# Performance work log

Hardware: AMD Instinct MI355X
Metric: run time of the kernel (lower is better)

The kernel has to match this reference:

```python
import jax, jax.numpy as jnp
import numpy as np
import math

BS, C, NH, NL, NP = 2, 128, 1, 2, 8
SHAPES = np.array([[128, 256], [64, 128]], dtype=np.int64)  # [num_level, (H, W)]
NQ = int(SHAPES[0, 0] * SHAPES[0, 1])  # 32768 queries at level-0 resolution
NV = int((SHAPES[:, 0] * SHAPES[:, 1]).sum())  # 40960


def _offset_bias():
    # replicate init_weights grid bias
    thetas = np.arange(NH, dtype=np.float32) * (2.0 * math.pi / NH)
    grid = np.stack([np.cos(thetas), np.sin(thetas)], -1)
    grid = grid / np.abs(grid).max(-1, keepdims=True)
    grid = np.tile(grid.reshape(NH, 1, 1, 2), (1, NL, NP, 1))
    for i in range(NP):
        grid[:, :, i, :] *= i + 1
    return jnp.asarray(grid.reshape(-1), dtype=jnp.float32)


def setup_inputs() -> dict:
    key = jax.random.key(0)
    ks = jax.random.split(key, 8)
    query = jax.random.normal(ks[0], (BS, NQ, C), dtype=jnp.float32)
    value = jax.random.normal(ks[1], (BS, NV, C), dtype=jnp.float32)
    query_location = jax.random.uniform(ks[2], (BS, NQ, NL, 2), dtype=jnp.float32)
    spatial_shapes = jnp.asarray(SHAPES)
    level_start_index = jnp.asarray(np.concatenate([[0], np.cumsum(SHAPES[:, 0] * SHAPES[:, 1])[:-1]]))
    # params (small random offset weights instead of exact-zero init so offsets depend on query)
    W_off = 0.01 * jax.random.normal(ks[3], (C, NH * NL * NP * 2), dtype=jnp.float32)
    b_off = _offset_bias()
    W_attn = 0.01 * jax.random.normal(ks[4], (C, NH * NL * NP), dtype=jnp.float32)
    b_attn = jnp.zeros((NH * NL * NP,), dtype=jnp.float32)
    lim = 1.0 / np.sqrt(C)
    W_out = jax.random.uniform(ks[5], (C * NH, C), minval=-lim, maxval=lim, dtype=jnp.float32)
    b_out = jnp.zeros((C,), dtype=jnp.float32)
    return {"query": query, "value": value, "query_location": query_location,
            "spatial_shapes": spatial_shapes, "level_start_index": level_start_index,
            "W_off": W_off, "b_off": b_off, "W_attn": W_attn, "b_attn": b_attn,
            "W_out": W_out, "b_out": b_out}


def _ms_deform_attn(value, shapes_np, loc, aw):
    # value: [bs, nv, c]; loc: [bs, nq, nh, nl, np, 2] in [0,1]; aw: [bs, nq, nh, nl, np]
    bs, nq = loc.shape[0], loc.shape[1]
    hd = value.shape[-1] // NH
    out = jnp.zeros((bs, NH, nq, hd), dtype=value.dtype)
    start = 0
    for l in range(NL):
        H, W = int(shapes_np[l, 0]), int(shapes_np[l, 1])
        # [bs, nh, H*W, hd]
        v = value[:, start:start + H * W].reshape(bs, H * W, NH, hd).transpose(0, 2, 1, 3)
        # grid_sample align_corners=False convention: x = gx*W - 0.5 with gx in [0,1]
        x = loc[:, :, :, l, :, 0] * W - 0.5  # [bs, nq, nh, np]
        y = loc[:, :, :, l, :, 1] * H - 0.5
        x0 = jnp.floor(x); y0 = jnp.floor(y)
        lx = (x - x0).transpose(0, 2, 1, 3).reshape(bs, NH, nq * NP)[..., None]
        ly = (y - y0).transpose(0, 2, 1, 3).reshape(bs, NH, nq * NP)[..., None]
        x0i = x0.astype(jnp.int32); y0i = y0.astype(jnp.int32)

        def gat(ix, iy):
            valid = ((ix >= 0) & (ix < W) & (iy >= 0) & (iy < H)).astype(value.dtype)
            idx = jnp.clip(iy, 0, H - 1) * W + jnp.clip(ix, 0, W - 1)
            idx_t = idx.transpose(0, 2, 1, 3).reshape(bs, NH, nq * NP)
            g = jnp.take_along_axis(v, idx_t[..., None], axis=2)  # [bs, nh, nq*np, hd]
            m = valid.transpose(0, 2, 1, 3).reshape(bs, NH, nq * NP)
            return g * m[..., None]

        samp = (gat(x0i, y0i) * (1 - lx) * (1 - ly)
                + gat(x0i + 1, y0i) * lx * (1 - ly)
                + gat(x0i, y0i + 1) * (1 - lx) * ly
                + gat(x0i + 1, y0i + 1) * lx * ly)  # [bs, nh, nq*np, hd]
        w = aw[:, :, :, l].transpose(0, 2, 1, 3).reshape(bs, NH, nq * NP)[..., None]
        out = out + (samp * w).reshape(bs, NH, nq, NP, hd).sum(3)
        start += H * W
    return out.transpose(0, 2, 1, 3).reshape(bs, nq, NH * hd)


def reference(query, value, query_location, spatial_shapes, level_start_index,
              W_off, b_off, W_attn, b_attn, W_out, b_out):
    bs, nq, c = query.shape
    shapes_np = np.asarray(spatial_shapes)
    off = (query @ W_off + b_off).reshape(bs, nq, NH, NL, NP, 2)
    aw = jax.nn.softmax((query @ W_attn + b_attn).reshape(bs, nq, NH, NL * NP), axis=-1)
    aw = aw.reshape(bs, nq, NH, NL, NP)
    # offset_normalizer = [W, H] per level
    norm = jnp.stack([jnp.asarray(shapes_np[:, 1], jnp.float32),
                      jnp.asarray(shapes_np[:, 0], jnp.float32)], -1)  # [nl, 2]
    loc = query_location[:, :, None, :, None, :] + off / norm[None, None, None, :, None, :]
    out = _ms_deform_attn(value, shapes_np, loc, aw)
    return out @ W_out + b_out  # dropout is identity at eval
```

## Files before the change

### kernel.cpp

```cpp
#include <hip/hip_runtime.h>


#define QB 32

__global__ __launch_bounds__(256, 4) void msda_gather_kernel(
    const float* __restrict__ query,
    const float* __restrict__ value,
    const float* __restrict__ qloc,
    const float* __restrict__ Woff,
    const float* __restrict__ boff,
    const float* __restrict__ Wattn,
    const float* __restrict__ battn,
    float* __restrict__ acc_out)
{
    __shared__ __align__(16) char smem_u[QB * 128 * 4];
    __shared__ float coords[QB * 32];
    __shared__ float aws[QB * 16];

    float*  q_tile = (float*)smem_u;
    float4* wo_w   = (float4*)smem_u;
    int4*   wo_o   = (int4*)(smem_u + QB * 16 * 16);

    const int tid = threadIdx.x;
    const int r0  = blockIdx.x * QB;

    {
        const float4* src = (const float4*)query + (size_t)r0 * 32;
        float4* dst = (float4*)q_tile;
        #pragma unroll
        for (int i = 0; i < 4; ++i)
            dst[tid + i * 256] = src[tid + i * 256];
    }
    __syncthreads();

    {
        const int jo = tid & 31;
        const int qb = (tid >> 5) * 4;
        float s[4] = {0.f, 0.f, 0.f, 0.f};
        for (int c4 = 0; c4 < 32; ++c4) {
            const float w0 = Woff[(c4 * 4 + 0) * 32 + jo];
            const float w1 = Woff[(c4 * 4 + 1) * 32 + jo];
            const float w2 = Woff[(c4 * 4 + 2) * 32 + jo];
            const float w3 = Woff[(c4 * 4 + 3) * 32 + jo];
            #pragma unroll
            for (int k = 0; k < 4; ++k) {
                const float4 q4 = *(const float4*)&q_tile[(qb + k) * 128 + c4 * 4];
                s[k] += q4.x * w0 + q4.y * w1 + q4.z * w2 + q4.w * w3;
            }
        }
        const int l = jo >> 4;
        const int d = jo & 1;
        const float scale = (d == 0) ? (l == 0 ? 256.f : 128.f)
                                     : (l == 0 ? 128.f : 64.f);
        const float bo = boff[jo];
        #pragma unroll
        for (int k = 0; k < 4; ++k) {
            const int row = r0 + qb + k;
            const float ql = qloc[row * 4 + l * 2 + d];
            coords[(qb + k) * 32 + jo] = ql * scale + (s[k] + bo) - 0.5f;
        }
    }

    {
        const int ja = tid & 15;
        const int qb = (tid >> 4) * 2;
        float s[2] = {0.f, 0.f};
        for (int c4 = 0; c4 < 32; ++c4) {
            const float w0 = Wattn[(c4 * 4 + 0) * 16 + ja];
            const float w1 = Wattn[(c4 * 4 + 1) * 16 + ja];
            const float w2 = Wattn[(c4 * 4 + 2) * 16 + ja];
            const float w3 = Wattn[(c4 * 4 + 3) * 16 + ja];
            #pragma unroll
            for (int k = 0; k < 2; ++k) {
                const float4 q4 = *(const float4*)&q_tile[(qb + k) * 128 + c4 * 4];
                s[k] += q4.x * w0 + q4.y * w1 + q4.z * w2 + q4.w * w3;
            }
        }
        const float ba = battn[ja];
        #pragma unroll
        for (int k = 0; k < 2; ++k)
            aws[(qb + k) * 16 + ja] = s[k] + ba;
    }
    __syncthreads();

    if (tid < QB) {
        float* a = &aws[tid * 16];
        float m = a[0];
        #pragma unroll
        for (int j = 1; j < 16; ++j) m = fmaxf(m, a[j]);
        float sum = 0.f;
        #pragma unroll
        for (int j = 0; j < 16; ++j) {
            const float e = __expf(a[j] - m);
            a[j] = e;
            sum += e;
        }
        const float r = 1.f / sum;
        #pragma unroll
        for (int j = 0; j < 16; ++j) a[j] *= r;
    }
    __syncthreads();

    #pragma unroll
    for (int e = tid; e < QB * 16; e += 256) {
        const int q = e >> 4;
        const int p = e & 15;
        const int l = p >> 3;
        const int H = l ? 64 : 128;
        const int W = l ? 128 : 256;
        const int S = l ? 32768 : 0;
        const float x   = coords[q * 32 + p * 2 + 0];
        const float y   = coords[q * 32 + p * 2 + 1];
        const float wgt = aws[q * 16 + p];
        const float xf = floorf(x), yf = floorf(y);
        const float lx = x - xf, ly = y - yf;
        const int x0 = (int)xf, y0 = (int)yf;
        const int x1 = x0 + 1, y1 = y0 + 1;
        const float hx = 1.f - lx, hy = 1.f - ly;
        float w00 = wgt * hx * hy;
        float w10 = wgt * lx * hy;
        float w01 = wgt * hx * ly;
        float w11 = wgt * lx * ly;
        if (x0 < 0 || x0 >= W) { w00 = 0.f; w01 = 0.f; }
        if (x1 < 0 || x1 >= W) { w10 = 0.f; w11 = 0.f; }
        if (y0 < 0 || y0 >= H) { w00 = 0.f; w10 = 0.f; }
        if (y1 < 0 || y1 >= H) { w01 = 0.f; w11 = 0.f; }
        const int cx0 = min(max(x0, 0), W - 1);
        const int cx1 = min(max(x1, 0), W - 1);
        const int cy0 = min(max(y0, 0), H - 1);
        const int cy1 = min(max(y1, 0), H - 1);
        wo_w[e] = make_float4(w00, w10, w01, w11);
        wo_o[e] = make_int4((S + cy0 * W + cx0) * 32,
                            (S + cy0 * W + cx1) * 32,
                            (S + cy1 * W + cx0) * 32,
                            (S + cy1 * W + cx1) * 32);
    }
    __syncthreads();

    {
        const int wv   = tid >> 6;
        const int lane = tid & 63;
        const int half = lane >> 5;
        const int cl   = lane & 31;
        const float4* vb = (const float4*)value
                         + (size_t)(blockIdx.x >> 10) * (40960 * 32);
        float4* og = (float4*)acc_out;

        #pragma unroll 1
        for (int i = 0; i < 8; ++i) {
            const int q = wv * 8 + i;
            const int base_e = q * 16;
            float ax = 0.f, ay = 0.f, az = 0.f, aw4 = 0.f;

            #pragma unroll 1
            for (int p0 = 0; p0 < 16; p0 += 8) {
                int   oa[8], ob[8];
                float wa[8], wb[8];
                #pragma unroll
                for (int pi = 0; pi < 8; ++pi) {
                    const float4 w = wo_w[base_e + p0 + pi];
                    const int4   o = wo_o[base_e + p0 + pi];
                    oa[pi] = (half ? o.y : o.x) + cl;
                    ob[pi] = (half ? o.w : o.z) + cl;
                    wa[pi] = half ? w.y : w.x;
                    wb[pi] = half ? w.w : w.z;
                }
                float4 vA[8], vB[8];
                #pragma unroll
                for (int pi = 0; pi < 8; ++pi) {
                    vA[pi] = vb[oa[pi]];
                    vB[pi] = vb[ob[pi]];
                }
                #pragma unroll
                for (int pi = 0; pi < 8; ++pi) {
                    ax  += wa[pi] * vA[pi].x + wb[pi] * vB[pi].x;
                    ay  += wa[pi] * vA[pi].y + wb[pi] * vB[pi].y;
                    az  += wa[pi] * vA[pi].z + wb[pi] * vB[pi].z;
                    aw4 += wa[pi] * vA[pi].w + wb[pi] * vB[pi].w;
                }
            }
            ax  += __shfl_xor(ax, 32, 64);
            ay  += __shfl_xor(ay, 32, 64);
            az  += __shfl_xor(az, 32, 64);
            aw4 += __shfl_xor(aw4, 32, 64);
            if (half == 0)
                og[(size_t)(r0 + q) * 32 + cl] = make_float4(ax, ay, az, aw4);
        }
    }
}

#define GR 64

__global__ __launch_bounds__(256, 3) void msda_out_gemm_kernel(
    const float* __restrict__ Wout,
    const float* __restrict__ bout,
    float* __restrict__ out)
{
    __shared__ __align__(16) float a_tile[GR * 68];
    __shared__ __align__(16) float w_tile[64 * 128];
    const int tid  = threadIdx.x;
    const int r0   = blockIdx.x * GR;
    const int trow = tid >> 4;
    const int tcol = tid & 15;

    float4 o[4][2];
    #pragma unroll
    for (int k = 0; k < 4; ++k) {
        o[k][0] = make_float4(0.f, 0.f, 0.f, 0.f);
        o[k][1] = make_float4(0.f, 0.f, 0.f, 0.f);
    }

    #pragma unroll 1
    for (int h = 0; h < 2; ++h) {
        {
            const float4* src = (const float4*)out;
            #pragma unroll
            for (int i = 0; i < 4; ++i) {
                const int t  = tid + i * 256;
                const int r  = t >> 4;
                const int c4 = t & 15;
                const float4 v = src[(size_t)(r0 + r) * 32 + h * 16 + c4];
                *(float4*)&a_tile[r * 68 + c4 * 4] = v;
            }
            const float4* ws = (const float4*)Wout + (size_t)h * 64 * 32;
            float4* wd = (float4*)w_tile;
            #pragma unroll
            for (int i = 0; i < 8; ++i)
                wd[tid + i * 256] = ws[tid + i * 256];
        }
        __syncthreads();

        #pragma unroll 1
        for (int c4 = 0; c4 < 16; ++c4) {
            float4 a4[4];
            #pragma unroll
            for (int k = 0; k < 4; ++k)
                a4[k] = *(const float4*)&a_tile[(trow + 16 * k) * 68 + c4 * 4];
            #pragma unroll
            for (int j = 0; j < 4; ++j) {
                const int ci = c4 * 4 + j;
                const float4 w0 = *(const float4*)&w_tile[ci * 128 + tcol * 8];
                const float4 w1 = *(const float4*)&w_tile[ci * 128 + tcol * 8 + 4];
                #pragma unroll
                for (int k = 0; k < 4; ++k) {
                    const float a = (j == 0) ? a4[k].x : (j == 1) ? a4[k].y
                                  : (j == 2) ? a4[k].z : a4[k].w;
                    o[k][0].x += a * w0.x; o[k][0].y += a * w0.y;
                    o[k][0].z += a * w0.z; o[k][0].w += a * w0.w;
                    o[k][1].x += a * w1.x; o[k][1].y += a * w1.y;
                    o[k][1].z += a * w1.z; o[k][1].w += a * w1.w;
                }
            }
        }
        __syncthreads();
    }

    const float4 b0 = ((const float4*)bout)[tcol * 2];
    const float4 b1 = ((const float4*)bout)[tcol * 2 + 1];
    float4* og = (float4*)out;
    #pragma unroll
    for (int k = 0; k < 4; ++k) {
        const size_t row = (size_t)(r0 + trow + 16 * k);
        float4 v0 = o[k][0], v1 = o[k][1];
        v0.x += b0.x; v0.y += b0.y; v0.z += b0.z; v0.w += b0.w;
        v1.x += b1.x; v1.y += b1.y; v1.z += b1.z; v1.w += b1.w;
        og[row * 32 + tcol * 2]     = v0;
        og[row * 32 + tcol * 2 + 1] = v1;
    }
}

extern "C" void kernel_launch(void* const* d_in, const int* in_sizes, int n_in,
                              void* d_out, int out_size, void* d_ws, size_t ws_size,
                              hipStream_t stream) {
    const float* query = (const float*)d_in[0];
    const float* value = (const float*)d_in[1];
    const float* qloc  = (const float*)d_in[2];
    const float* Woff  = (const float*)d_in[5];
    const float* boff  = (const float*)d_in[6];
    const float* Wattn = (const float*)d_in[7];
    const float* battn = (const float*)d_in[8];
    const float* Wout  = (const float*)d_in[9];
    const float* bout  = (const float*)d_in[10];
    float* out = (float*)d_out;

    hipLaunchKernelGGL(msda_gather_kernel, dim3(65536 / QB), dim3(256), 0, stream,
                       query, value, qloc, Woff, boff, Wattn, battn, out);
    hipLaunchKernelGGL(msda_out_gemm_kernel, dim3(65536 / GR), dim3(256), 0, stream,
                       Wout, bout, out);
}
```

Measured before the change: 274.8 us.

## Convert value tensor to fp16 in workspace and gather half-precision samples

Adds a pre-pass kernel that converts the value tensor to fp16 in the workspace. A new gather kernel reads 8-byte half4 samples instead of 16-byte float4, and issues all 16 points' loads up front before accumulating in fp32. The goal is to halve gather bandwidth and cache footprint and to improve memory-level parallelism. It costs an extra conversion pass over the value tensor each call, adds fp16 rounding error, and raises register pressure. The old fp32 path is kept as a fallback when the workspace is too small.

```diff
diff --git a/kernel.cpp b/kernel.cpp
--- a/kernel.cpp
+++ b/kernel.cpp
@@ -1,9 +1,207 @@
 #include <hip/hip_runtime.h>
+#include <hip/hip_fp16.h>
 
 
 #define QB 32
 
-__global__ __launch_bounds__(256, 4) void msda_gather_kernel(
+struct __align__(8) h2x2 { __half2 a, b; };
+
+__global__ __launch_bounds__(256) void cvt_value_f16_kernel(
+    const float4* __restrict__ in, h2x2* __restrict__ out, int n4)
+{
+    const int i = blockIdx.x * 256 + threadIdx.x;
+    if (i < n4) {
+        const float4 f = in[i];
+        h2x2 h;
+        h.a = __floats2half2_rn(f.x, f.y);
+        h.b = __floats2half2_rn(f.z, f.w);
+        out[i] = h;
+    }
+}
+
+#define MSDA_PROLOGUE                                                          \
+    float*  q_tile = (float*)smem_u;                                           \
+    float4* wo_w   = (float4*)smem_u;                                          \
+    int4*   wo_o   = (int4*)(smem_u + QB * 16 * 16);                           \
+    const int tid = threadIdx.x;                                               \
+    const int r0  = blockIdx.x * QB;                                           \
+    {                                                                          \
+        const float4* src = (const float4*)query + (size_t)r0 * 32;            \
+        float4* dst = (float4*)q_tile;                                         \
+        _Pragma("unroll")                                                      \
+        for (int i = 0; i < 4; ++i)                                            \
+            dst[tid + i * 256] = src[tid + i * 256];                           \
+    }                                                                          \
+    __syncthreads();                                                           \
+    {                                                                          \
+        const int jo = tid & 31;                                               \
+        const int qb = (tid >> 5) * 4;                                         \
+        float s[4] = {0.f, 0.f, 0.f, 0.f};                                     \
+        for (int c4 = 0; c4 < 32; ++c4) {                                      \
+            const float w0 = Woff[(c4 * 4 + 0) * 32 + jo];                     \
+            const float w1 = Woff[(c4 * 4 + 1) * 32 + jo];                     \
+            const float w2 = Woff[(c4 * 4 + 2) * 32 + jo];                     \
+            const float w3 = Woff[(c4 * 4 + 3) * 32 + jo];                     \
+            _Pragma("unroll")                                                  \
+            for (int k = 0; k < 4; ++k) {                                      \
+                const float4 q4 = *(const float4*)&q_tile[(qb + k) * 128 + c4 * 4]; \
+                s[k] += q4.x * w0 + q4.y * w1 + q4.z * w2 + q4.w * w3;         \
+            }                                                                  \
+        }                                                                      \
+        const int l = jo >> 4;                                                 \
+        const int d = jo & 1;                                                  \
+        const float scale = (d == 0) ? (l == 0 ? 256.f : 128.f)                \
+                                     : (l == 0 ? 128.f : 64.f);                \
+        const float bo = boff[jo];                                             \
+        _Pragma("unroll")                                                      \
+        for (int k = 0; k < 4; ++k) {                                          \
+            const int row = r0 + qb + k;                                       \
+            const float ql = qloc[row * 4 + l * 2 + d];                        \
+            coords[(qb + k) * 32 + jo] = ql * scale + (s[k] + bo) - 0.5f;      \
+        }                                                                      \
+    }                                                                          \
+    {                                                                          \
+        const int ja = tid & 15;                                               \
+        const int qb = (tid >> 4) * 2;                                         \
+        float s[2] = {0.f, 0.f};                                               \
+        for (int c4 = 0; c4 < 32; ++c4) {                                      \
+            const float w0 = Wattn[(c4 * 4 + 0) * 16 + ja];                    \
+            const float w1 = Wattn[(c4 * 4 + 1) * 16 + ja];                    \
+            const float w2 = Wattn[(c4 * 4 + 2) * 16 + ja];                    \
+            const float w3 = Wattn[(c4 * 4 + 3) * 16 + ja];                    \
+            _Pragma("unroll")                                                  \
+            for (int k = 0; k < 2; ++k) {                                      \
+                const float4 q4 = *(const float4*)&q_tile[(qb + k) * 128 + c4 * 4]; \
+                s[k] += q4.x * w0 + q4.y * w1 + q4.z * w2 + q4.w * w3;         \
+            }                                                                  \
+        }                                                                      \
+        const float ba = battn[ja];                                            \
+        _Pragma("unroll")                                                      \
+        for (int k = 0; k < 2; ++k)                                            \
+            aws[(qb + k) * 16 + ja] = s[k] + ba;                               \
+    }                                                                          \
+    __syncthreads();                                                           \
+    if (tid < QB) {                                                            \
+        float* a = &aws[tid * 16];                                             \
+        float m = a[0];                                                        \
+        _Pragma("unroll")                                                      \
+        for (int j = 1; j < 16; ++j) m = fmaxf(m, a[j]);                       \
+        float sum = 0.f;                                                       \
+        _Pragma("unroll")                                                      \
+        for (int j = 0; j < 16; ++j) {                                         \
+            const float e = __expf(a[j] - m);                                  \
+            a[j] = e;                                                          \
+            sum += e;                                                          \
+        }                                                                      \
+        const float r = 1.f / sum;                                             \
+        _Pragma("unroll")                                                      \
+        for (int j = 0; j < 16; ++j) a[j] *= r;                                \
+    }                                                                          \
+    __syncthreads();                                                           \
+    _Pragma("unroll")                                                          \
+    for (int e = tid; e < QB * 16; e += 256) {                                 \
+        const int q = e >> 4;                                                  \
+        const int p = e & 15;                                                  \
+        const int l = p >> 3;                                                  \
+        const int H = l ? 64 : 128;                                            \
+        const int W = l ? 128 : 256;                                           \
+        const int S = l ? 32768 : 0;                                           \
+        const float x   = coords[q * 32 + p * 2 + 0];                          \
+        const float y   = coords[q * 32 + p * 2 + 1];                          \
+        const float wgt = aws[q * 16 + p];                                     \
+        const float xf = floorf(x), yf = floorf(y);                            \
+        const float lx = x - xf, ly = y - yf;                                  \
+        const int x0 = (int)xf, y0 = (int)yf;                                  \
+        const int x1 = x0 + 1, y1 = y0 + 1;                                    \
+        const float hx = 1.f - lx, hy = 1.f - ly;                              \
+        float w00 = wgt * hx * hy;                                             \
+        float w10 = wgt * lx * hy;                                             \
+        float w01 = wgt * hx * ly;                                             \
+        float w11 = wgt * lx * ly;                                             \
+        if (x0 < 0 || x0 >= W) { w00 = 0.f; w01 = 0.f; }                       \
+        if (x1 < 0 || x1 >= W) { w10 = 0.f; w11 = 0.f; }                       \
+        if (y0 < 0 || y0 >= H) { w00 = 0.f; w10 = 0.f; }                       \
+        if (y1 < 0 || y1 >= H) { w01 = 0.f; w11 = 0.f; }                       \
+        const int cx0 = min(max(x0, 0), W - 1);                                \
+        const int cx1 = min(max(x1, 0), W - 1);                                \
+        const int cy0 = min(max(y0, 0), H - 1);                                \
+        const int cy1 = min(max(y1, 0), H - 1);                                \
+        wo_w[e] = make_float4(w00, w10, w01, w11);                             \
+        wo_o[e] = make_int4((S + cy0 * W + cx0) * 32,                          \
+                            (S + cy0 * W + cx1) * 32,                          \
+                            (S + cy1 * W + cx0) * 32,                          \
+                            (S + cy1 * W + cx1) * 32);                        \
+    }                                                                          \
+    __syncthreads();
+
+__global__ __launch_bounds__(256, 4) void msda_gather_f16_kernel(
+    const float* __restrict__ query,
+    const h2x2*  __restrict__ value_h,
+    const float* __restrict__ qloc,
+    const float* __restrict__ Woff,
+    const float* __restrict__ boff,
+    const float* __restrict__ Wattn,
+    const float* __restrict__ battn,
+    float* __restrict__ acc_out)
+{
+    __shared__ __align__(16) char smem_u[QB * 128 * 4];
+    __shared__ float coords[QB * 32];
+    __shared__ float aws[QB * 16];
+    MSDA_PROLOGUE
+
+    {
+        const int wv   = tid >> 6;
+        const int lane = tid & 63;
+        const int half = lane >> 5;
+        const int cl   = lane & 31;
+        const h2x2* vb = value_h + (size_t)(blockIdx.x >> 10) * (40960 * 32);
+        float4* og = (float4*)acc_out;
+
+        #pragma unroll 1
+        for (int i = 0; i < 8; ++i) {
+            const int q = wv * 8 + i;
+            const int base_e = q * 16;
+            float ax = 0.f, ay = 0.f, az = 0.f, aw4 = 0.f;
+
+            int   oa[16], ob[16];
+            float wa[16], wb[16];
+            #pragma unroll
+            for (int p = 0; p < 16; ++p) {
+                const float4 w = wo_w[base_e + p];
+                const int4   o = wo_o[base_e + p];
+                oa[p] = (half ? o.y : o.x) + cl;
+                ob[p] = (half ? o.w : o.z) + cl;
+                wa[p] = half ? w.y : w.x;
+                wb[p] = half ? w.w : w.z;
+            }
+            h2x2 vA[16], vB[16];
+            #pragma unroll
+            for (int p = 0; p < 16; ++p) {
+                vA[p] = vb[oa[p]];
+                vB[p] = vb[ob[p]];
+            }
+            #pragma unroll
+            for (int p = 0; p < 16; ++p) {
+                const float2 a0 = __half22float2(vA[p].a);
+                const float2 a1 = __half22float2(vA[p].b);
+                const float2 b0 = __half22float2(vB[p].a);
+                const float2 b1 = __half22float2(vB[p].b);
+                ax  += wa[p] * a0.x + wb[p] * b0.x;
+                ay  += wa[p] * a0.y + wb[p] * b0.y;
+                az  += wa[p] * a1.x + wb[p] * b1.x;
+                aw4 += wa[p] * a1.y + wb[p] * b1.y;
+            }
+            ax  += __shfl_xor(ax, 32, 64);
+            ay  += __shfl_xor(ay, 32, 64);
+            az  += __shfl_xor(az, 32, 64);
+            aw4 += __shfl_xor(aw4, 32, 64);
+            if (half == 0)
+                og[(size_t)(r0 + q) * 32 + cl] = make_float4(ax, ay, az, aw4);
+        }
+    }
+}
+
+__global__ __launch_bounds__(256, 4) void msda_gather_f32_kernel(
     const float* __restrict__ query,
     const float* __restrict__ value,
     const float* __restrict__ qloc,
@@ -16,126 +214,7 @@
     __shared__ __align__(16) char smem_u[QB * 128 * 4];
     __shared__ float coords[QB * 32];
     __shared__ float aws[QB * 16];
-
-    float*  q_tile = (float*)smem_u;
-    float4* wo_w   = (float4*)smem_u;
-    int4*   wo_o   = (int4*)(smem_u + QB * 16 * 16);
-
-    const int tid = threadIdx.x;
-    const int r0  = blockIdx.x * QB;
-
-    {
-        const float4* src = (const float4*)query + (size_t)r0 * 32;
-        float4* dst = (float4*)q_tile;
-        #pragma unroll
-        for (int i = 0; i < 4; ++i)
-            dst[tid + i * 256] = src[tid + i * 256];
-    }
-    __syncthreads();
-
-    {
-        const int jo = tid & 31;
-        const int qb = (tid >> 5) * 4;
-        float s[4] = {0.f, 0.f, 0.f, 0.f};
-        for (int c4 = 0; c4 < 32; ++c4) {
-            const float w0 = Woff[(c4 * 4 + 0) * 32 + jo];
-            const float w1 = Woff[(c4 * 4 + 1) * 32 + jo];
-            const float w2 = Woff[(c4 * 4 + 2) * 32 + jo];
-            const float w3 = Woff[(c4 * 4 + 3) * 32 + jo];
-            #pragma unroll
-            for (int k = 0; k < 4; ++k) {
-                const float4 q4 = *(const float4*)&q_tile[(qb + k) * 128 + c4 * 4];
-                s[k] += q4.x * w0 + q4.y * w1 + q4.z * w2 + q4.w * w3;
-            }
-        }
-        const int l = jo >> 4;
-        const int d = jo & 1;
-        const float scale = (d == 0) ? (l == 0 ? 256.f : 128.f)
-                                     : (l == 0 ? 128.f : 64.f);
-        const float bo = boff[jo];
-        #pragma unroll
-        for (int k = 0; k < 4; ++k) {
-            const int row = r0 + qb + k;
-            const float ql = qloc[row * 4 + l * 2 + d];
-            coords[(qb + k) * 32 + jo] = ql * scale + (s[k] + bo) - 0.5f;
-        }
-    }
-
-    {
-        const int ja = tid & 15;
-        const int qb = (tid >> 4) * 2;
-        float s[2] = {0.f, 0.f};
-        for (int c4 = 0; c4 < 32; ++c4) {
-            const float w0 = Wattn[(c4 * 4 + 0) * 16 + ja];
-            const float w1 = Wattn[(c4 * 4 + 1) * 16 + ja];
-            const float w2 = Wattn[(c4 * 4 + 2) * 16 + ja];
-            const float w3 = Wattn[(c4 * 4 + 3) * 16 + ja];
-            #pragma unroll
-            for (int k = 0; k < 2; ++k) {
-                const float4 q4 = *(const float4*)&q_tile[(qb + k) * 128 + c4 * 4];
-                s[k] += q4.x * w0 + q4.y * w1 + q4.z * w2 + q4.w * w3;
-            }
-        }
-        const float ba = battn[ja];
-        #pragma unroll
-        for (int k = 0; k < 2; ++k)
-            aws[(qb + k) * 16 + ja] = s[k] + ba;
-    }
-    __syncthreads();
-
-    if (tid < QB) {
-        float* a = &aws[tid * 16];
-        float m = a[0];
-        #pragma unroll
-        for (int j = 1; j < 16; ++j) m = fmaxf(m, a[j]);
-        float sum = 0.f;
-        #pragma unroll
-        for (int j = 0; j < 16; ++j) {
-            const float e = __expf(a[j] - m);
-            a[j] = e;
-            sum += e;
-        }
-        const float r = 1.f / sum;
-        #pragma unroll
-        for (int j = 0; j < 16; ++j) a[j] *= r;
-    }
-    __syncthreads();
-
-    #pragma unroll
-    for (int e = tid; e < QB * 16; e += 256) {
-        const int q = e >> 4;
-        const int p = e & 15;
-        const int l = p >> 3;
-        const int H = l ? 64 : 128;
-        const int W = l ? 128 : 256;
-        const int S = l ? 32768 : 0;
-        const float x   = coords[q * 32 + p * 2 + 0];
-        const float y   = coords[q * 32 + p * 2 + 1];
-        const float wgt = aws[q * 16 + p];
-        const float xf = floorf(x), yf = floorf(y);
-        const float lx = x - xf, ly = y - yf;
-        const int x0 = (int)xf, y0 = (int)yf;
-        const int x1 = x0 + 1, y1 = y0 + 1;
-        const float hx = 1.f - lx, hy = 1.f - ly;
-        float w00 = wgt * hx * hy;
-        float w10 = wgt * lx * hy;
-        float w01 = wgt * hx * ly;
-        float w11 = wgt * lx * ly;
-        if (x0 < 0 || x0 >= W) { w00 = 0.f; w01 = 0.f; }
-        if (x1 < 0 || x1 >= W) { w10 = 0.f; w11 = 0.f; }
-        if (y0 < 0 || y0 >= H) { w00 = 0.f; w10 = 0.f; }
-        if (y1 < 0 || y1 >= H) { w01 = 0.f; w11 = 0.f; }
-        const int cx0 = min(max(x0, 0), W - 1);
-        const int cx1 = min(max(x1, 0), W - 1);
-        const int cy0 = min(max(y0, 0), H - 1);
-        const int cy1 = min(max(y1, 0), H - 1);
-        wo_w[e] = make_float4(w00, w10, w01, w11);
-        wo_o[e] = make_int4((S + cy0 * W + cx0) * 32,
-                            (S + cy0 * W + cx1) * 32,
-                            (S + cy1 * W + cx0) * 32,
-                            (S + cy1 * W + cx1) * 32);
-    }
-    __syncthreads();
+    MSDA_PROLOGUE
 
     {
         const int wv   = tid >> 6;
@@ -283,8 +362,22 @@
     const float* bout  = (const float*)d_in[10];
     float* out = (float*)d_out;
 
-    hipLaunchKernelGGL(msda_gather_kernel, dim3(65536 / QB), dim3(256), 0, stream,
-                       query, value, qloc, Woff, boff, Wattn, battn, out);
+    const int n_val = 2 * 40960 * 128;
+    const size_t f16_bytes = (size_t)n_val * 2;
+
+    if (ws_size >= f16_bytes) {
+        h2x2* val16 = (h2x2*)d_ws;
+        const int n4 = n_val / 4;
+        hipLaunchKernelGGL(cvt_value_f16_kernel, dim3((n4 + 255) / 256), dim3(256),
+                           0, stream, (const float4*)value, val16, n4);
+        hipLaunchKernelGGL(msda_gather_f16_kernel, dim3(65536 / QB), dim3(256),
+                           0, stream,
+                           query, (const h2x2*)val16, qloc, Woff, boff, Wattn, battn, out);
+    } else {
+        hipLaunchKernelGGL(msda_gather_f32_kernel, dim3(65536 / QB), dim3(256),
+                           0, stream,
+                           query, value, qloc, Woff, boff, Wattn, battn, out);
+    }
     hipLaunchKernelGGL(msda_out_gemm_kernel, dim3(65536 / GR), dim3(256), 0, stream,
                        Wout, bout, out);
 }
```

Measured after the change: 243.7 us. 11.3% less time.
